# Performance work log

Measured on AMD Instinct MI355X. Metric: run time of the kernel, lower is better.

The kernel has to match this reference:

```python
import jax, jax.numpy as jnp
import numpy as np

N, E = 50000, 800000
IN_C, H_C, OUT_C, HEADS = 64, 32, 32, 8


def setup_inputs() -> dict:
    key = jax.random.key(0)
    ks = jax.random.split(key, 16)
    def glorot(k, shape):
        fan_in = shape[-1]
        return jax.random.normal(k, shape, dtype=jnp.float32) / jnp.sqrt(jnp.float32(fan_in))
    inp = {
        'x': jax.random.normal(ks[0], (N, IN_C), dtype=jnp.float32),
        'edge_index': jax.random.randint(ks[1], (2, E), 0, N, dtype=jnp.int64),
        # layer 1: in_c -> h_c, heads
        'W1l': glorot(ks[2], (HEADS * H_C, IN_C)),
        'b1l': jnp.zeros((HEADS * H_C,), jnp.float32),
        'W1r': glorot(ks[3], (HEADS * H_C, IN_C)),
        'b1r': jnp.zeros((HEADS * H_C,), jnp.float32),
        'att1': glorot(ks[4], (HEADS, H_C)),
        'bias1': jnp.zeros((H_C,), jnp.float32),
        # layer 2: h_c -> out_c, heads
        'W2l': glorot(ks[5], (HEADS * OUT_C, H_C)),
        'b2l': jnp.zeros((HEADS * OUT_C,), jnp.float32),
        'W2r': glorot(ks[6], (HEADS * OUT_C, H_C)),
        'b2r': jnp.zeros((HEADS * OUT_C,), jnp.float32),
        'att2': glorot(ks[7], (HEADS, OUT_C)),
        'bias2': jnp.zeros((OUT_C,), jnp.float32),
    }
    return inp


def _gatv2_layer(x, src, dst, valid, Wl, bl, Wr, br, att, bias):
    # PyG GATv2Conv (share_weights=False, concat=False): message j->i uses
    # e = att . leaky_relu(lin_l(x_j) + lin_r(x_i), 0.2); softmax over dst; agg lin_l(x_j).
    n = x.shape[0]
    heads, c = att.shape
    xl = (x @ Wl.T + bl).reshape(n, heads, c)
    xr = (x @ Wr.T + br).reshape(n, heads, c)
    m = jax.nn.leaky_relu(xl[src] + xr[dst], negative_slope=0.2)  # [Etot,H,C]
    score = jnp.einsum('ehc,hc->eh', m, att)                      # [Etot,H]
    score = jnp.where(valid[:, None], score, -jnp.inf)
    smax = jax.ops.segment_max(score, dst, num_segments=n)        # [N,H]
    a = jnp.where(valid[:, None], jnp.exp(score - smax[dst]), 0.0)
    denom = jax.ops.segment_sum(a, dst, num_segments=n)
    a = a / jnp.maximum(denom[dst], 1e-16)
    out = jax.ops.segment_sum(a[..., None] * xl[src], dst, num_segments=n)  # [N,H,C]
    return out.mean(axis=1) + bias


def reference(x, edge_index, W1l, b1l, W1r, b1r, att1, bias1,
              W2l, b2l, W2r, b2r, att2, bias2):
    n = x.shape[0]
    src0, dst0 = edge_index[0], edge_index[1]
    # PyG removes existing self loops then adds fresh ones: mask originals,
    # append one self loop per node (keeps static shapes).
    loop = jnp.arange(n, dtype=src0.dtype)
    src = jnp.concatenate([src0, loop])
    dst = jnp.concatenate([dst0, loop])
    valid = jnp.concatenate([src0 != dst0, jnp.ones((n,), bool)])
    h = _gatv2_layer(x, src, dst, valid, W1l, b1l, W1r, b1r, att1, bias1)
    h = jax.nn.leaky_relu(h, negative_slope=0.01)  # nn.LeakyReLU default
    out = _gatv2_layer(h, src, dst, valid, W2l, b2l, W2r, b2r, att2, bias2)
    return out
```

## Files before the change

kernel.cpp:

```cpp
#include <hip/hip_runtime.h>
#include <math.h>

#define HEADS 8
#define CDIM 32
#define ODIM 256

typedef _Float16 h2 __attribute__((ext_vector_type(2)));
typedef _Float16 h4 __attribute__((ext_vector_type(4)));
union H4 { h4 v; h2 p[2]; };

#if __has_builtin(__builtin_amdgcn_fdot2)
#define FDOT2(a,b,c) __builtin_amdgcn_fdot2((a),(b),(c),false)
#else
static __device__ __forceinline__ float fdot2_sw(h2 a, h2 b, float c){
  return fmaf((float)a.x, (float)b.x, fmaf((float)a.y, (float)b.y, c));
}
#define FDOT2(a,b,c) fdot2_sw((a),(b),(c))
#endif

__device__ __forceinline__ float lrelu(float v, float s){ return fmaxf(v, s*v); }

__global__ void block_sum_kernel(const int* __restrict__ counts, int* __restrict__ bsums, int n){
  int i = blockIdx.x*256 + threadIdx.x;
  int v = (i < n) ? counts[i] : 0;
#pragma unroll
  for (int off=1; off<64; off<<=1) v += __shfl_xor(v, off);
  __shared__ int ws[4];
  int lane = threadIdx.x & 63, w = threadIdx.x >> 6;
  if (lane == 0) ws[w] = v;
  __syncthreads();
  if (threadIdx.x == 0) bsums[blockIdx.x] = ws[0]+ws[1]+ws[2]+ws[3];
}

__global__ __launch_bounds__(1024) void scan_bsums_kernel(int* __restrict__ bsums, int nb){
  __shared__ int s[1024];
  int t = threadIdx.x;
  int v = (t < nb) ? bsums[t] : 0;
  s[t] = v;
  __syncthreads();
  for (int off=1; off<1024; off<<=1){
    int u = (t >= off) ? s[t-off] : 0;
    __syncthreads();
    s[t] += u;
    __syncthreads();
  }
  if (t < nb) bsums[t] = s[t] - v;
}

__global__ void local_scan_kernel(const int* __restrict__ counts, const int* __restrict__ bsums,
                                  int* __restrict__ indptr, int n){
  __shared__ int s[256];
  int t = threadIdx.x;
  int i = blockIdx.x*256 + t;
  int v = (i < n) ? counts[i] : 0;
  s[t] = v;
  __syncthreads();
  for (int off=1; off<256; off<<=1){
    int u = (t >= off) ? s[t-off] : 0;
    __syncthreads();
    s[t] += u;
    __syncthreads();
  }
  int excl = s[t] - v + bsums[blockIdx.x];
  if (i < n) indptr[i] = excl;
  if (i == n-1) indptr[n] = excl + v;
}

__global__ void scatter_kernel(const int* __restrict__ src, const int* __restrict__ dst,
                               const int* __restrict__ rank, const int* __restrict__ indptr,
                               int* __restrict__ csr_src, int e){
  int i = blockIdx.x*256 + threadIdx.x;
  if (i < e){
    int r = rank[i];
    if (r >= 0){
      int d = dst[i];
      csr_src[indptr[d] + r] = src[i];
    }
  }
}

template<int K, bool FUSE_COUNT>
__global__ __launch_bounds__(256, 2) void gemm_kernel(const float* __restrict__ X,
    const float* __restrict__ Wl, const float* __restrict__ bl,
    const float* __restrict__ Wr, const float* __restrict__ br,
    _Float16* __restrict__ outl, _Float16* __restrict__ outr, int n,
    const int* __restrict__ src, const int* __restrict__ dst,
    int* __restrict__ counts, int* __restrict__ rank, int e){
  if (FUSE_COUNT && blockIdx.y == 0){
    const int CB = 96;
    if (blockIdx.x < CB){
      int stride = CB*256;
      for (int i = blockIdx.x*256 + threadIdx.x; i < e; i += stride){
        int s = src[i], d = dst[i];
        int r = -1;
        if (s != d) r = atomicAdd(counts + d, 1);
        rank[i] = r;
      }
    }
    return;
  }
  const int KP = K + 4;
  __shared__ float xt[128*(K+4)];
  __shared__ float wt[2][64*(K+4)];
  int t = threadIdx.x;
  int n0 = blockIdx.x*128;
  int o0 = (FUSE_COUNT ? (blockIdx.y-1) : blockIdx.y)*64;

  for (int idx = t; idx < 128*(K/4); idx += 256){
    int row = idx/(K/4), c = (idx%(K/4))*4;
    int node = n0 + row; if (node >= n) node = n-1;
    *(float4*)(xt + row*KP + c) = *(const float4*)(X + (size_t)node*K + c);
  }
  for (int idx = t; idx < 64*(K/4); idx += 256){
    int row = idx/(K/4), c = (idx%(K/4))*4;
    *(float4*)(wt[0] + row*KP + c) = *(const float4*)(Wl + (size_t)(o0+row)*K + c);
    *(float4*)(wt[1] + row*KP + c) = *(const float4*)(Wr + (size_t)(o0+row)*K + c);
  }
  __syncthreads();

  int og = t & 15;
  int ng = t >> 4;
  float accl[8][4] = {{0.f}}, accr[8][4] = {{0.f}};

#pragma unroll 2
  for (int kk = 0; kk < K; kk += 4){
    float4 xv[8], wl4[4], wr4[4];
#pragma unroll
    for (int i=0;i<8;i++) xv[i] = *(const float4*)(xt + (ng+16*i)*KP + kk);
#pragma unroll
    for (int j=0;j<4;j++){
      wl4[j] = *(const float4*)(wt[0] + (og+16*j)*KP + kk);
      wr4[j] = *(const float4*)(wt[1] + (og+16*j)*KP + kk);
    }
#pragma unroll
    for (int i=0;i<8;i++){
#pragma unroll
      for (int j=0;j<4;j++){
        accl[i][j] = fmaf(xv[i].x, wl4[j].x, fmaf(xv[i].y, wl4[j].y,
                     fmaf(xv[i].z, wl4[j].z, fmaf(xv[i].w, wl4[j].w, accl[i][j]))));
        accr[i][j] = fmaf(xv[i].x, wr4[j].x, fmaf(xv[i].y, wr4[j].y,
                     fmaf(xv[i].z, wr4[j].z, fmaf(xv[i].w, wr4[j].w, accr[i][j]))));
      }
    }
  }

  float bvl[4], bvr[4];
#pragma unroll
  for (int j=0;j<4;j++){ bvl[j] = bl[o0+og+16*j]; bvr[j] = br[o0+og+16*j]; }
#pragma unroll
  for (int i=0;i<8;i++){
    int node = n0 + ng + 16*i;
    if (node < n){
      _Float16* pl = outl + (size_t)node*ODIM + o0 + og;
      _Float16* pr = outr + (size_t)node*ODIM + o0 + og;
#pragma unroll
      for (int j=0;j<4;j++){
        pl[16*j] = (_Float16)(accl[i][j] + bvl[j]);
        pr[16*j] = (_Float16)(accr[i][j] + bvr[j]);
      }
    }
  }
}

__global__ __launch_bounds__(256) void edge_kernel(
    const _Float16* __restrict__ xl, const _Float16* __restrict__ xr,
    const float* __restrict__ att, const float* __restrict__ bias,
    const int* __restrict__ indptr, const int* __restrict__ csr_src,
    float* __restrict__ out, int n, int act)
{
  int wid = blockIdx.x*4 + (threadIdx.x >> 6);
  if (wid >= n) return;
  int lane = threadIdx.x & 63;
  const float LOG2E = 1.44269504088896341f;

  float4 attf = *(const float4*)(att + 4*lane);
  h2 at0 = (h2){(_Float16)(attf.x*LOG2E), (_Float16)(attf.y*LOG2E)};
  h2 at1 = (h2){(_Float16)(attf.z*LOG2E), (_Float16)(attf.w*LOG2E)};
  const h2 c02 = {(_Float16)0.2f, (_Float16)0.2f};

  H4 xrh; xrh.v = *(const h4*)(xr + (size_t)wid*ODIM + 4*lane);
  H4 self; self.v = *(const h4*)(xl + (size_t)wid*ODIM + 4*lane);

  auto score = [&](const H4& c)->float{
    h2 t0 = c.p[0] + xrh.p[0];
    h2 t1 = c.p[1] + xrh.p[1];
    h2 q0 = __builtin_elementwise_max(t0, t0 * c02);
    h2 q1 = __builtin_elementwise_max(t1, t1 * c02);
    float d = FDOT2(q0, at0, FDOT2(q1, at1, 0.f));
    d += __shfl_xor(d, 1);
    d += __shfl_xor(d, 2);
    d += __shfl_xor(d, 4);
    return d;
  };

  float w0 = exp2f(score(self));
  float denom = w0;
  float4 acc;
  acc.x = w0 * (float)self.v.x;
  acc.y = w0 * (float)self.v.y;
  acc.z = w0 * (float)self.v.z;
  acc.w = w0 * (float)self.v.w;

  int beg = __builtin_amdgcn_readfirstlane(indptr[wid]);
  int end = __builtin_amdgcn_readfirstlane(indptr[wid+1]);
  int cnt = end - beg;
  H4 r0, r1;
  r0.v = (h4){}; r1.v = (h4){};
  if (cnt > 0){
    int s0 = __builtin_amdgcn_readfirstlane(csr_src[beg]);
    r0.v = *(const h4*)(xl + (size_t)s0*ODIM + 4*lane);
  }
  if (cnt > 1){
    int s1 = __builtin_amdgcn_readfirstlane(csr_src[beg+1]);
    r1.v = *(const h4*)(xl + (size_t)s1*ODIM + 4*lane);
  }
  for (int k = 0; k < cnt; ++k){
    H4 cur = r0; r0 = r1;
    if (k+2 < cnt){
      int s2 = __builtin_amdgcn_readfirstlane(csr_src[beg+k+2]);
      r1.v = *(const h4*)(xl + (size_t)s2*ODIM + 4*lane);
    }
    float pe = exp2f(score(cur));
    denom += pe;
    acc.x = fmaf(pe, (float)cur.v.x, acc.x);
    acc.y = fmaf(pe, (float)cur.v.y, acc.y);
    acc.z = fmaf(pe, (float)cur.v.z, acc.z);
    acc.w = fmaf(pe, (float)cur.v.w, acc.w);
  }
  float inv = 1.f/denom;
  float vx = acc.x*inv, vy = acc.y*inv, vz = acc.z*inv, vw = acc.w*inv;
  vx += __shfl_xor(vx, 8);  vx += __shfl_xor(vx, 16);  vx += __shfl_xor(vx, 32);
  vy += __shfl_xor(vy, 8);  vy += __shfl_xor(vy, 16);  vy += __shfl_xor(vy, 32);
  vz += __shfl_xor(vz, 8);  vz += __shfl_xor(vz, 16);  vz += __shfl_xor(vz, 32);
  vw += __shfl_xor(vw, 8);  vw += __shfl_xor(vw, 16);  vw += __shfl_xor(vw, 32);
  if (lane < 8){
    float4 bv = *(const float4*)(bias + 4*lane);
    float ox = vx*0.125f + bv.x;
    float oy = vy*0.125f + bv.y;
    float oz = vz*0.125f + bv.z;
    float ow = vw*0.125f + bv.w;
    if (act){
      ox = lrelu(ox, 0.01f); oy = lrelu(oy, 0.01f);
      oz = lrelu(oz, 0.01f); ow = lrelu(ow, 0.01f);
    }
    *(float4*)(out + (size_t)wid*CDIM + 4*lane) = make_float4(ox, oy, oz, ow);
  }
}

extern "C" void kernel_launch(void* const* d_in, const int* in_sizes, int n_in,
                              void* d_out, int out_size, void* d_ws, size_t ws_size,
                              hipStream_t stream){
  (void)n_in; (void)out_size; (void)ws_size;
  const float* x    = (const float*)d_in[0];
  const int*   ei   = (const int*)d_in[1];
  const float* W1l  = (const float*)d_in[2];
  const float* b1l  = (const float*)d_in[3];
  const float* W1r  = (const float*)d_in[4];
  const float* b1r  = (const float*)d_in[5];
  const float* att1 = (const float*)d_in[6];
  const float* bias1= (const float*)d_in[7];
  const float* W2l  = (const float*)d_in[8];
  const float* b2l  = (const float*)d_in[9];
  const float* W2r  = (const float*)d_in[10];
  const float* b2r  = (const float*)d_in[11];
  const float* att2 = (const float*)d_in[12];
  const float* bias2= (const float*)d_in[13];
  int n = in_sizes[0] / 64;
  int e = in_sizes[1] / 2;
  const int* src = ei;
  const int* dst = ei + e;

  char* ws = (char*)d_ws;
  size_t off = 0;
  auto alloc = [&](size_t bytes)->char*{
    char* p = ws + off; off += (bytes + 255) & ~(size_t)255; return p;
  };
  _Float16* xl  = (_Float16*)alloc((size_t)n*ODIM*2);
  _Float16* xr  = (_Float16*)alloc((size_t)n*ODIM*2);
  float* h      = (float*)alloc((size_t)n*CDIM*4);
  int*   counts = (int*)alloc((size_t)n*4);
  int*   indptr = (int*)alloc((size_t)(n+1)*4);
  int*   rank   = (int*)alloc((size_t)e*4);
  int*   csr    = (int*)alloc((size_t)e*4);
  int*   bsums  = (int*)alloc((size_t)1024*4);

  int nblk = (n + 255) / 256;
  int ntiles = (n + 127) / 128;
  hipMemsetAsync(counts, 0, (size_t)n*4, stream);

  gemm_kernel<64,true><<<dim3(ntiles,5), 256, 0, stream>>>(
      x, W1l, b1l, W1r, b1r, xl, xr, n, src, dst, counts, rank, e);
  block_sum_kernel<<<nblk, 256, 0, stream>>>(counts, bsums, n);
  scan_bsums_kernel<<<1, 1024, 0, stream>>>(bsums, nblk);
  local_scan_kernel<<<nblk, 256, 0, stream>>>(counts, bsums, indptr, n);
  scatter_kernel<<<(e+255)/256, 256, 0, stream>>>(src, dst, rank, indptr, csr, e);

  edge_kernel<<<(n+3)/4, 256, 0, stream>>>(xl, xr, att1, bias1, indptr, csr, h, n, 1);
  gemm_kernel<32,false><<<dim3(ntiles,4), 256, 0, stream>>>(
      h, W2l, b2l, W2r, b2r, xl, xr, n, nullptr, nullptr, nullptr, nullptr, 0);
  edge_kernel<<<(n+3)/4, 256, 0, stream>>>(xl, xr, att2, bias2, indptr, csr, (float*)d_out, n, 0);
}
```

Before: 329.3 us.

## Replace FP32 FMA projection GEMM with fp16 MFMA kernel

```diff
diff --git a/kernel.cpp b/kernel.cpp
--- a/kernel.cpp
+++ b/kernel.cpp
@@ -7,6 +7,8 @@
 
 typedef _Float16 h2 __attribute__((ext_vector_type(2)));
 typedef _Float16 h4 __attribute__((ext_vector_type(4)));
+typedef _Float16 h8 __attribute__((ext_vector_type(8)));
+typedef float f32x4 __attribute__((ext_vector_type(4)));
 union H4 { h4 v; h2 p[2]; };
 
 #if __has_builtin(__builtin_amdgcn_fdot2)
@@ -80,83 +82,84 @@
 }
 
 template<int K, bool FUSE_COUNT>
-__global__ __launch_bounds__(256, 2) void gemm_kernel(const float* __restrict__ X,
+__global__ __launch_bounds__(256, 2) void gemm_mfma(const float* __restrict__ X,
     const float* __restrict__ Wl, const float* __restrict__ bl,
     const float* __restrict__ Wr, const float* __restrict__ br,
     _Float16* __restrict__ outl, _Float16* __restrict__ outr, int n,
     const int* __restrict__ src, const int* __restrict__ dst,
     int* __restrict__ counts, int* __restrict__ rank, int e){
   if (FUSE_COUNT && blockIdx.y == 0){
-    const int CB = 96;
-    if (blockIdx.x < CB){
-      int stride = CB*256;
-      for (int i = blockIdx.x*256 + threadIdx.x; i < e; i += stride){
-        int s = src[i], d = dst[i];
-        int r = -1;
-        if (s != d) r = atomicAdd(counts + d, 1);
-        rank[i] = r;
-      }
+    int stride = gridDim.x*256;
+    for (int i = blockIdx.x*256 + threadIdx.x; i < e; i += stride){
+      int s = src[i], d = dst[i];
+      int r = -1;
+      if (s != d) r = atomicAdd(counts + d, 1);
+      rank[i] = r;
     }
     return;
   }
-  const int KP = K + 4;
-  __shared__ float xt[128*(K+4)];
-  __shared__ float wt[2][64*(K+4)];
+  const int KP = K + 8;
+  __shared__ __align__(16) _Float16 Xs[64*(K+8)];
   int t = threadIdx.x;
-  int n0 = blockIdx.x*128;
-  int o0 = (FUSE_COUNT ? (blockIdx.y-1) : blockIdx.y)*64;
-
-  for (int idx = t; idx < 128*(K/4); idx += 256){
+  int n0 = blockIdx.x*64;
+  int ybase = FUSE_COUNT ? (blockIdx.y-1) : blockIdx.y;
+
+  for (int idx = t; idx < 64*(K/4); idx += 256){
     int row = idx/(K/4), c = (idx%(K/4))*4;
     int node = n0 + row; if (node >= n) node = n-1;
-    *(float4*)(xt + row*KP + c) = *(const float4*)(X + (size_t)node*K + c);
-  }
-  for (int idx = t; idx < 64*(K/4); idx += 256){
-    int row = idx/(K/4), c = (idx%(K/4))*4;
-    *(float4*)(wt[0] + row*KP + c) = *(const float4*)(Wl + (size_t)(o0+row)*K + c);
-    *(float4*)(wt[1] + row*KP + c) = *(const float4*)(Wr + (size_t)(o0+row)*K + c);
+    float4 xv = *(const float4*)(X + (size_t)node*K + c);
+    h4 hv = {(_Float16)xv.x, (_Float16)xv.y, (_Float16)xv.z, (_Float16)xv.w};
+    *(h4*)(Xs + row*KP + c) = hv;
   }
   __syncthreads();
 
-  int og = t & 15;
-  int ng = t >> 4;
-  float accl[8][4] = {{0.f}}, accr[8][4] = {{0.f}};
-
-#pragma unroll 2
-  for (int kk = 0; kk < K; kk += 4){
-    float4 xv[8], wl4[4], wr4[4];
-#pragma unroll
-    for (int i=0;i<8;i++) xv[i] = *(const float4*)(xt + (ng+16*i)*KP + kk);
-#pragma unroll
-    for (int j=0;j<4;j++){
-      wl4[j] = *(const float4*)(wt[0] + (og+16*j)*KP + kk);
-      wr4[j] = *(const float4*)(wt[1] + (og+16*j)*KP + kk);
-    }
-#pragma unroll
-    for (int i=0;i<8;i++){
-#pragma unroll
-      for (int j=0;j<4;j++){
-        accl[i][j] = fmaf(xv[i].x, wl4[j].x, fmaf(xv[i].y, wl4[j].y,
-                     fmaf(xv[i].z, wl4[j].z, fmaf(xv[i].w, wl4[j].w, accl[i][j]))));
-        accr[i][j] = fmaf(xv[i].x, wr4[j].x, fmaf(xv[i].y, wr4[j].y,
-                     fmaf(xv[i].z, wr4[j].z, fmaf(xv[i].w, wr4[j].w, accr[i][j]))));
-      }
-    }
-  }
-
-  float bvl[4], bvr[4];
-#pragma unroll
-  for (int j=0;j<4;j++){ bvl[j] = bl[o0+og+16*j]; bvr[j] = br[o0+og+16*j]; }
-#pragma unroll
-  for (int i=0;i<8;i++){
-    int node = n0 + ng + 16*i;
-    if (node < n){
-      _Float16* pl = outl + (size_t)node*ODIM + o0 + og;
-      _Float16* pr = outr + (size_t)node*ODIM + o0 + og;
-#pragma unroll
-      for (int j=0;j<4;j++){
-        pl[16*j] = (_Float16)(accl[i][j] + bvl[j]);
-        pr[16*j] = (_Float16)(accr[i][j] + bvr[j]);
+  int wave = t >> 6, lane = t & 63;
+  int co = ybase*256 + wave*64;
+  const float* W   = (co < 256) ? Wl : Wr;
+  const float* Bv  = (co < 256) ? bl : br;
+  _Float16* outp   = (co < 256) ? outl : outr;
+  int lco = co & 255;
+  int lr = lane & 15, lg = lane >> 4;
+
+  f32x4 acc[4][4];
+#pragma unroll
+  for (int c = 0; c < 4; ++c)
+#pragma unroll
+    for (int m = 0; m < 4; ++m) acc[c][m] = (f32x4){0.f, 0.f, 0.f, 0.f};
+
+#pragma unroll
+  for (int ks = 0; ks < K/32; ++ks){
+    int k0 = ks*32 + lg*8;
+    h8 a[4], b[4];
+#pragma unroll
+    for (int c = 0; c < 4; ++c){
+      const float* wp = W + (size_t)(lco + c*16 + lr)*K + k0;
+      float4 w0 = *(const float4*)(wp);
+      float4 w1 = *(const float4*)(wp + 4);
+      a[c] = (h8){(_Float16)w0.x,(_Float16)w0.y,(_Float16)w0.z,(_Float16)w0.w,
+                  (_Float16)w1.x,(_Float16)w1.y,(_Float16)w1.z,(_Float16)w1.w};
+    }
+#pragma unroll
+    for (int m = 0; m < 4; ++m)
+      b[m] = *(const h8*)(Xs + (m*16 + lr)*KP + k0);
+#pragma unroll
+    for (int c = 0; c < 4; ++c)
+#pragma unroll
+      for (int m = 0; m < 4; ++m)
+        acc[c][m] = __builtin_amdgcn_mfma_f32_16x16x32_f16(a[c], b[m], acc[c][m], 0, 0, 0);
+  }
+
+#pragma unroll
+  for (int c = 0; c < 4; ++c){
+    int ch = lco + c*16 + lg*4;
+    float4 bb = *(const float4*)(Bv + ch);
+#pragma unroll
+    for (int m = 0; m < 4; ++m){
+      int node = n0 + m*16 + lr;
+      if (node < n){
+        h4 o = {(_Float16)(acc[c][m][0] + bb.x), (_Float16)(acc[c][m][1] + bb.y),
+                (_Float16)(acc[c][m][2] + bb.z), (_Float16)(acc[c][m][3] + bb.w)};
+        *(h4*)(outp + (size_t)node*ODIM + ch) = o;
       }
     }
   }
@@ -285,10 +288,10 @@
   int*   bsums  = (int*)alloc((size_t)1024*4);
 
   int nblk = (n + 255) / 256;
-  int ntiles = (n + 127) / 128;
+  int nt64 = (n + 63) / 64;
   hipMemsetAsync(counts, 0, (size_t)n*4, stream);
 
-  gemm_kernel<64,true><<<dim3(ntiles,5), 256, 0, stream>>>(
+  gemm_mfma<64,true><<<dim3(nt64,3), 256, 0, stream>>>(
       x, W1l, b1l, W1r, b1r, xl, xr, n, src, dst, counts, rank, e);
   block_sum_kernel<<<nblk, 256, 0, stream>>>(counts, bsums, n);
   scan_bsums_kernel<<<1, 1024, 0, stream>>>(bsums, nblk);
@@ -296,7 +299,7 @@
   scatter_kernel<<<(e+255)/256, 256, 0, stream>>>(src, dst, rank, indptr, csr, e);
 
   edge_kernel<<<(n+3)/4, 256, 0, stream>>>(xl, xr, att1, bias1, indptr, csr, h, n, 1);
-  gemm_kernel<32,false><<<dim3(ntiles,4), 256, 0, stream>>>(
+  gemm_mfma<32,false><<<dim3(nt64,2), 256, 0, stream>>>(
       h, W2l, b2l, W2r, b2r, xl, xr, n, nullptr, nullptr, nullptr, nullptr, 0);
   edge_kernel<<<(n+3)/4, 256, 0, stream>>>(xl, xr, att2, bias2, indptr, csr, (float*)d_out, n, 0);
 }
```

Result: slower. 337.1 us (+2.4%).
